# Kernel optimization log

Measured on AMD Instinct MI355X. Metric: run time of the kernel, lower is better.

## Reference

```python
import jax, jax.numpy as jnp
import numpy as np

D_MODEL = 2048
N_HEAD = 16
HEAD_DIM = D_MODEL // N_HEAD
FF_MULT = 4
LN_EPS = 1e-5


def layer_norm(x, w, b):
    mu = jnp.mean(x, axis=-1, keepdims=True)
    var = jnp.mean(jnp.square(x - mu), axis=-1, keepdims=True)
    return (x - mu) * jax.lax.rsqrt(var + LN_EPS) * w + b


def setup_inputs() -> dict:
    key = jax.random.key(0)
    ks = jax.random.split(key, 10)
    B, S, D = 2, 2048, D_MODEL
    s = 1.0 / np.sqrt(D)
    inp = {
        "x": jax.random.normal(ks[0], (B, S, D), jnp.float32),
        "token_emb": jax.random.normal(ks[1], (B, S, D), jnp.float32),
        # torch Linear weights are (out_features, in_features)
        "Wq": jax.random.normal(ks[2], (D, D), jnp.float32) * s,
        "Wk": jax.random.normal(ks[3], (D, D), jnp.float32) * s,
        "Wv": jax.random.normal(ks[4], (D, D), jnp.float32) * s,
        "Wo": jax.random.normal(ks[5], (D, D), jnp.float32) * s,
        "W1": jax.random.normal(ks[6], (FF_MULT * D, D), jnp.float32) * s,
        "W2": jax.random.normal(ks[7], (D, FF_MULT * D), jnp.float32) * (1.0 / np.sqrt(FF_MULT * D)),
        "ln1_w": jnp.ones((D,), jnp.float32),
        "ln1_b": jnp.zeros((D,), jnp.float32),
        "ln2_w": jnp.ones((D,), jnp.float32),
        "ln2_b": jnp.zeros((D,), jnp.float32),
    }
    return inp


def reference(x, token_emb, Wq, Wk, Wv, Wo, W1, W2, ln1_w, ln1_b, ln2_w, ln2_b):
    B, S, D = x.shape
    H, Hd = N_HEAD, HEAD_DIM

    h_norm = layer_norm(x, ln1_w, ln1_b)
    # torch Linear: y = x @ W.T
    q = (h_norm @ Wq.T).reshape(B, S, H, Hd).transpose(0, 2, 1, 3)  # (B,H,S,Hd)
    k = (h_norm @ Wk.T).reshape(B, S, H, Hd).transpose(0, 2, 1, 3)
    v = (token_emb @ Wv.T).reshape(B, S, H, Hd).transpose(0, 2, 1, 3)

    scores = jnp.einsum("bhqd,bhkd->bhqk", q, k) / np.sqrt(Hd)
    causal = jnp.tril(jnp.ones((S, S), bool))  # (S,S)
    scores = jnp.where(causal, scores, -jnp.inf)
    weights = jax.nn.softmax(scores, axis=-1)

    attn = jnp.einsum("bhqk,bhkd->bhqd", weights, v)
    attn = attn.transpose(0, 2, 1, 3).reshape(B, S, D)
    attn = attn @ Wo.T
    x = x + attn

    h_ffn = layer_norm(x, ln2_w, ln2_b)
    ffn = jax.nn.gelu(h_ffn @ W1.T, approximate=False) @ W2.T
    return x + ffn
```

## Files before the change

kernel.cpp:

```cpp
#include <hip/hip_runtime.h>
#include <hip/hip_bf16.h>
#include <math.h>

#define D_MODEL 2048
#define SEQ     2048
#define BATCH   2
#define NTOK    (BATCH*SEQ)
#define NHEAD   16
#define HDIM    128
#define FF      8192

typedef float  f32x4  __attribute__((ext_vector_type(4)));
typedef __bf16 bf16x8 __attribute__((ext_vector_type(8)));

__device__ __forceinline__ unsigned short f2bfbits(float f) {
    unsigned u = __builtin_bit_cast(unsigned, f);
    return (unsigned short)((u + 0x7fffu + ((u >> 16) & 1u)) >> 16);
}
__device__ __forceinline__ __bf16 f2bf(float f) {
    unsigned short h = f2bfbits(f);
    return __builtin_bit_cast(__bf16, h);
}

__device__ __forceinline__ void gld_lds16(const void* g, void* l) {
    __builtin_amdgcn_global_load_lds(
        (const __attribute__((address_space(1))) unsigned int*)g,
        (__attribute__((address_space(3))) unsigned int*)l, 16, 0, 0);
}

__global__ __launch_bounds__(256) void cvt_all(
        const float* __restrict__ tok, const float* __restrict__ wq,
        const float* __restrict__ wk,  const float* __restrict__ wv,
        const float* __restrict__ wo,  const float* __restrict__ w1,
        const float* __restrict__ w2,
        __bf16* __restrict__ tokb, __bf16* __restrict__ wqb,
        __bf16* __restrict__ wkb,  __bf16* __restrict__ wvb,
        __bf16* __restrict__ wob,  __bf16* __restrict__ w1b,
        __bf16* __restrict__ w2b) {
    const size_t M4 = 4u * 1024 * 1024;
    size_t i = (size_t)blockIdx.x * 1024 + (size_t)threadIdx.x * 4;
    const float* src; __bf16* dst; size_t off;
    if      (i < 2*M4)  { src = tok; dst = tokb; off = i; }
    else if (i < 3*M4)  { src = wq;  dst = wqb;  off = i - 2*M4; }
    else if (i < 4*M4)  { src = wk;  dst = wkb;  off = i - 3*M4; }
    else if (i < 5*M4)  { src = wv;  dst = wvb;  off = i - 4*M4; }
    else if (i < 6*M4)  { src = wo;  dst = wob;  off = i - 5*M4; }
    else if (i < 10*M4) { src = w1;  dst = w1b;  off = i - 6*M4; }
    else                { src = w2;  dst = w2b;  off = i - 10*M4; }
    float4 v = *(const float4*)(src + off);
    ushort4 o;
    o.x = f2bfbits(v.x); o.y = f2bfbits(v.y);
    o.z = f2bfbits(v.z); o.w = f2bfbits(v.w);
    *(ushort4*)((unsigned short*)dst + off) = o;
}

__global__ __launch_bounds__(256) void add_reduce(
        const float* __restrict__ p0, const float* __restrict__ p1,
        const float* __restrict__ resid, float* __restrict__ out) {
    int i = blockIdx.x * 256 + threadIdx.x;
    float4 a = ((const float4*)p0)[i];
    float4 b = ((const float4*)p1)[i];
    float4 r = ((const float4*)resid)[i];
    float4 o;
    o.x = a.x + b.x + r.x; o.y = a.y + b.y + r.y;
    o.z = a.z + b.z + r.z; o.w = a.w + b.w + r.w;
    ((float4*)out)[i] = o;
}

__global__ __launch_bounds__(256) void ln_bf16(
        const float* __restrict__ x, const float* __restrict__ w,
        const float* __restrict__ b, __bf16* __restrict__ out) {
    const int row = blockIdx.x;
    const int tid = threadIdx.x;
    const float* xr = x + (size_t)row * D_MODEL;
    float4 v0 = *(const float4*)(xr + tid * 8);
    float4 v1 = *(const float4*)(xr + tid * 8 + 4);
    float va[8] = {v0.x, v0.y, v0.z, v0.w, v1.x, v1.y, v1.z, v1.w};
    float s = 0.f, ss = 0.f;
#pragma unroll
    for (int j = 0; j < 8; ++j) { s += va[j]; ss += va[j] * va[j]; }
#pragma unroll
    for (int m = 32; m; m >>= 1) { s += __shfl_xor(s, m, 64); ss += __shfl_xor(ss, m, 64); }
    __shared__ float red[8];
    const int wid = tid >> 6;
    if ((tid & 63) == 0) { red[wid * 2] = s; red[wid * 2 + 1] = ss; }
    __syncthreads();
    s  = red[0] + red[2] + red[4] + red[6];
    ss = red[1] + red[3] + red[5] + red[7];
    const float mu   = s * (1.0f / D_MODEL);
    const float var  = ss * (1.0f / D_MODEL) - mu * mu;
    const float rstd = rsqrtf(var + 1e-5f);
    const int c = tid * 8;
    ushort4 o0, o1;
    unsigned short ob[8];
#pragma unroll
    for (int j = 0; j < 8; ++j)
        ob[j] = f2bfbits((va[j] - mu) * rstd * w[c + j] + b[c + j]);
    o0.x = ob[0]; o0.y = ob[1]; o0.z = ob[2]; o0.w = ob[3];
    o1.x = ob[4]; o1.y = ob[5]; o1.z = ob[6]; o1.w = ob[7];
    ushort4* op = (ushort4*)(out + (size_t)row * D_MODEL + c);
    op[0] = o0; op[1] = o1;
}

template <int EPI, int SPLITK>
__global__ __launch_bounds__(512, 2) void gemm_bt8(
        const __bf16* __restrict__ A, const __bf16* __restrict__ Bm,
        __bf16* __restrict__ Cb, float* __restrict__ Cf,
        const float* __restrict__ resid, int M, int N, int K) {
    __shared__ __align__(16) __bf16 lds[2][2][256 * 64];
    const int tid = threadIdx.x;
    const int wid = tid >> 6, lane = tid & 63;
    const int l16 = lane & 15, lhi = lane >> 4;
    const int wm = wid >> 2, wn = wid & 3;

    int id = blockIdx.x;
    const int cpx = gridDim.x >> 3;
    id = (id & 7) * cpx + (id >> 3);
    const int nbn = N >> 8;
    int slice = 0;
    if (SPLITK == 2) {
        const int nblk = (M >> 8) * nbn;
        slice = id / nblk;
        id -= slice * nblk;
    }
    const int bm = id / nbn, bn = id % nbn;

    const __bf16* Ag = A  + (size_t)bm * 256 * K;
    const __bf16* Bg = Bm + (size_t)bn * 256 * K;
    const int tps = (K >> 6) / SPLITK;
    const int t0 = slice * tps, t1 = t0 + tps;

    auto stage = [&](__bf16* region, const __bf16* G, int kt, int half) {
#pragma unroll
        for (int j = 0; j < 2; ++j) {
            int idx = j * 512 + tid;
            int r128 = idx >> 3;
            int Xc = (idx & 7) << 4;
            int Xs = Xc ^ ((r128 & 7) << 4);
            gld_lds16((const char*)(G + ((size_t)(half * 128 + r128) * K + kt * 64)) + Xs,
                      (char*)region + half * 16384 + idx * 16);
        }
    };

    f32x4 acc[8][4] = {};
    bf16x8 af0[4][2], af1[4][2], bq0[2][2], bq1[2][2];

    const __bf16* Abase;
    const __bf16* Bbase;
    auto ldA = [&](bf16x8 (&dst)[4][2], int qm) {
#pragma unroll
        for (int i = 0; i < 4; ++i)
#pragma unroll
            for (int ks = 0; ks < 2; ++ks) {
                int r = wm * 128 + (qm * 4 + i) * 16 + l16;
                int X = ks * 64 + lhi * 16;
                dst[i][ks] = *(const bf16x8*)((const char*)Abase + r * 128 +
                                              (X ^ ((r & 7) << 4)));
            }
    };
    auto ldB = [&](bf16x8 (&dst)[2][2], int qn) {
#pragma unroll
        for (int j = 0; j < 2; ++j)
#pragma unroll
            for (int ks = 0; ks < 2; ++ks) {
                int r = wn * 64 + (qn * 2 + j) * 16 + l16;
                int X = ks * 64 + lhi * 16;
                dst[j][ks] = *(const bf16x8*)((const char*)Bbase + r * 128 +
                                              (X ^ ((r & 7) << 4)));
            }
    };
    auto mfmaQ = [&](bf16x8 (&a)[4][2], bf16x8 (&b)[2][2], int mo, int no) {
        __builtin_amdgcn_s_setprio(1);
#pragma unroll
        for (int i = 0; i < 4; ++i)
#pragma unroll
            for (int j = 0; j < 2; ++j)
#pragma unroll
                for (int ks = 0; ks < 2; ++ks)
                    acc[mo + i][no + j] = __builtin_amdgcn_mfma_f32_16x16x32_bf16(
                        a[i][ks], b[j][ks], acc[mo + i][no + j], 0, 0, 0);
        __builtin_amdgcn_s_setprio(0);
    };

    stage(&lds[0][0][0], Ag, t0, 0); stage(&lds[0][0][0], Ag, t0, 1);
    stage(&lds[0][1][0], Bg, t0, 0); stage(&lds[0][1][0], Bg, t0, 1);
    asm volatile("s_waitcnt vmcnt(0)" ::: "memory");
    __builtin_amdgcn_s_barrier();

    for (int t = t0; t < t1; ++t) {
        const int cur = (t - t0) & 1;
        Abase = &lds[cur][0][0];
        Bbase = &lds[cur][1][0];
        const bool pf = (t + 1 < t1);
        if (pf) {
            stage(&lds[cur ^ 1][0][0], Ag, t + 1, 0);
            stage(&lds[cur ^ 1][0][0], Ag, t + 1, 1);
            stage(&lds[cur ^ 1][1][0], Bg, t + 1, 0);
            stage(&lds[cur ^ 1][1][0], Bg, t + 1, 1);
        }
        ldA(af0, 0); ldB(bq0, 0);
        __builtin_amdgcn_s_barrier();
        asm volatile("s_waitcnt lgkmcnt(0)" ::: "memory");
        __builtin_amdgcn_sched_barrier(0);
        mfmaQ(af0, bq0, 0, 0);
        __builtin_amdgcn_s_barrier();
        ldB(bq1, 1);
        __builtin_amdgcn_s_barrier();
        asm volatile("s_waitcnt lgkmcnt(0)" ::: "memory");
        __builtin_amdgcn_sched_barrier(0);
        mfmaQ(af0, bq1, 0, 2);
        __builtin_amdgcn_s_barrier();
        ldA(af1, 1);
        __builtin_amdgcn_s_barrier();
        asm volatile("s_waitcnt lgkmcnt(0)" ::: "memory");
        __builtin_amdgcn_sched_barrier(0);
        mfmaQ(af1, bq0, 4, 0);
        __builtin_amdgcn_s_barrier();
        mfmaQ(af1, bq1, 4, 2);
        if (pf) asm volatile("s_waitcnt vmcnt(0)" ::: "memory");
        __builtin_amdgcn_s_barrier();
    }

#pragma unroll
    for (int m = 0; m < 8; ++m) {
        const int row = bm * 256 + wm * 128 + m * 16 + lhi * 4;
#pragma unroll
        for (int n = 0; n < 4; ++n) {
            const int col = bn * 256 + wn * 64 + n * 16 + l16;
            if (EPI == 3) {
                const int h = col >> 7, hd = col & 127;
                const size_t obase =
                    ((((size_t)(row >> 11) * NHEAD + h) * HDIM + hd) << 11) + (row & 2047);
                ushort4 o;
                o.x = f2bfbits(acc[m][n][0]); o.y = f2bfbits(acc[m][n][1]);
                o.z = f2bfbits(acc[m][n][2]); o.w = f2bfbits(acc[m][n][3]);
                *(ushort4*)((unsigned short*)Cb + obase) = o;
            } else {
#pragma unroll
                for (int r = 0; r < 4; ++r) {
                    float v = acc[m][n][r];
                    size_t off = (size_t)(row + r) * N + col;
                    if (EPI == 0) {
                        Cb[off] = f2bf(v);
                    } else if (EPI == 1) {
                        Cb[off] = f2bf(0.5f * v * (1.0f + erff(v * 0.70710678118654752f)));
                    } else if (EPI == 2) {
                        Cf[off] = v + resid[off];
                    } else {
                        Cf[(size_t)slice * M * N + off] = v;
                    }
                }
            }
        }
    }
}

#define LDQK 4096
__global__ __launch_bounds__(256) void attn_causal(
        const __bf16* __restrict__ Q, const __bf16* __restrict__ K,
        const __bf16* __restrict__ Vt, __bf16* __restrict__ O) {
    const int qt = gridDim.x - 1 - blockIdx.x;
    const int h = blockIdx.y, bb = blockIdx.z;
    const int tid = threadIdx.x, wid = tid >> 6, lane = tid & 63;
    const int l16 = lane & 15, lhi = lane >> 4;
    __shared__ __align__(16) __bf16 Ks[64 * 128];
    __shared__ __align__(16) __bf16 Vs[128 * 64];
    __shared__ __align__(16) __bf16 Pl[4][16 * 72];

    const size_t qkbase = ((size_t)bb * SEQ) * LDQK + (size_t)h * HDIM;
    const size_t obase  = ((size_t)bb * SEQ) * D_MODEL + (size_t)h * HDIM;
    const size_t vtbase = (((size_t)bb * NHEAD + h) * HDIM) << 11;
    const int q0 = qt * 64 + wid * 16;

    bf16x8 qf[4];
#pragma unroll
    for (int ks = 0; ks < 4; ++ks)
        qf[ks] = *(const bf16x8*)(Q + qkbase + (size_t)(q0 + l16) * LDQK + ks * 32 + lhi * 8);

    f32x4 accO[8] = {};
    float m_run[4], l_run[4];
#pragma unroll
    for (int r = 0; r < 4; ++r) { m_run[r] = -1e30f; l_run[r] = 0.f; }

    const float scale2 = 0.08838834764831845f * 1.4426950408889634f;

    for (int kt = 0; kt <= qt; ++kt) {
#pragma unroll
        for (int i = 0; i < 4; ++i) {
            int idx = i * 256 + tid;
            int row = idx >> 4, c8 = idx & 15;
            int c8s = c8 ^ (row & 7);
            gld_lds16(K + qkbase + (size_t)(kt * 64 + row) * LDQK + c8s * 8, Ks + idx * 8);
        }
#pragma unroll
        for (int i = 0; i < 4; ++i) {
            int idx = i * 256 + tid;
            int row = idx >> 3, c8 = idx & 7;
            int c8s = c8 ^ (row & 7);
            gld_lds16(Vt + vtbase + (size_t)row * SEQ + kt * 64 + c8s * 8, Vs + idx * 8);
        }
        __syncthreads();

        f32x4 s[4] = {};
        __builtin_amdgcn_s_setprio(1);
#pragma unroll
        for (int nb = 0; nb < 4; ++nb) {
            const int tok = nb * 16 + l16;
#pragma unroll
            for (int ks = 0; ks < 4; ++ks) {
                int co = (ks * 64 + lhi * 16) ^ ((tok & 7) << 4);
                bf16x8 kf = *(const bf16x8*)((const char*)Ks + tok * 256 + co);
                s[nb] = __builtin_amdgcn_mfma_f32_16x16x32_bf16(qf[ks], kf, s[nb], 0, 0, 0);
            }
        }
        __builtin_amdgcn_s_setprio(0);
        const bool diag = (kt == qt);
#pragma unroll
        for (int nb = 0; nb < 4; ++nb)
#pragma unroll
            for (int r = 0; r < 4; ++r) {
                float sv = s[nb][r] * scale2;
                if (diag && (nb * 16 + l16) > (wid * 16 + lhi * 4 + r)) sv = -1e30f;
                s[nb][r] = sv;
            }
        float alpha[4];
#pragma unroll
        for (int r = 0; r < 4; ++r) {
            float mx = fmaxf(fmaxf(s[0][r], s[1][r]), fmaxf(s[2][r], s[3][r]));
#pragma unroll
            for (int m = 8; m; m >>= 1) mx = fmaxf(mx, __shfl_xor(mx, m, 64));
            float mnew = fmaxf(m_run[r], mx);
            alpha[r] = exp2f(m_run[r] - mnew);
            float rs = 0.f;
#pragma unroll
            for (int nb = 0; nb < 4; ++nb) {
                float p = exp2f(s[nb][r] - mnew);
                s[nb][r] = p;
                rs += p;
            }
#pragma unroll
            for (int m = 8; m; m >>= 1) rs += __shfl_xor(rs, m, 64);
            l_run[r] = l_run[r] * alpha[r] + rs;
            m_run[r] = mnew;
        }
#pragma unroll
        for (int d8 = 0; d8 < 8; ++d8)
#pragma unroll
            for (int r = 0; r < 4; ++r) accO[d8][r] *= alpha[r];
#pragma unroll
        for (int nb = 0; nb < 4; ++nb)
#pragma unroll
            for (int r = 0; r < 4; ++r)
                Pl[wid][(lhi * 4 + r) * 72 + nb * 16 + l16] = f2bf(s[nb][r]);
        __builtin_amdgcn_s_setprio(1);
#pragma unroll
        for (int ks2 = 0; ks2 < 2; ++ks2) {
            bf16x8 pa = *(const bf16x8*)(&Pl[wid][l16 * 72 + ks2 * 32 + lhi * 8]);
#pragma unroll
            for (int d8 = 0; d8 < 8; ++d8) {
                const int d = d8 * 16 + l16;
                const int co = ((ks2 * 4 + lhi) ^ (d & 7)) << 4;
                bf16x8 vf = *(const bf16x8*)((const char*)Vs + d * 128 + co);
                accO[d8] = __builtin_amdgcn_mfma_f32_16x16x32_bf16(pa, vf, accO[d8], 0, 0, 0);
            }
        }
        __builtin_amdgcn_s_setprio(0);
        __syncthreads();
    }

#pragma unroll
    for (int d8 = 0; d8 < 8; ++d8)
#pragma unroll
        for (int r = 0; r < 4; ++r) {
            float o = accO[d8][r] / l_run[r];
            O[obase + (size_t)(q0 + lhi * 4 + r) * D_MODEL + d8 * 16 + l16] = f2bf(o);
        }
}

extern "C" void kernel_launch(void* const* d_in, const int* in_sizes, int n_in,
                              void* d_out, int out_size, void* d_ws, size_t ws_size,
                              hipStream_t stream) {
    const float* x    = (const float*)d_in[0];
    const float* tok  = (const float*)d_in[1];
    const float* Wq   = (const float*)d_in[2];
    const float* Wk   = (const float*)d_in[3];
    const float* Wv   = (const float*)d_in[4];
    const float* Wo   = (const float*)d_in[5];
    const float* W1   = (const float*)d_in[6];
    const float* W2   = (const float*)d_in[7];
    const float* ln1w = (const float*)d_in[8];
    const float* ln1b = (const float*)d_in[9];
    const float* ln2w = (const float*)d_in[10];
    const float* ln2b = (const float*)d_in[11];
    float* out = (float*)d_out;

    char* ws = (char*)d_ws;
    size_t off = 0;
    auto alloc = [&](size_t bytes) { void* p = ws + off; off += bytes; return p; };
    __bf16* tokb  = (__bf16*)alloc((size_t)NTOK * D_MODEL * 2);
    __bf16* hnorm = (__bf16*)alloc((size_t)NTOK * D_MODEL * 2);
    __bf16* wqb   = (__bf16*)alloc((size_t)D_MODEL * D_MODEL * 2);
    __bf16* wkb   = (__bf16*)alloc((size_t)D_MODEL * D_MODEL * 2);
    __bf16* wvb   = (__bf16*)alloc((size_t)D_MODEL * D_MODEL * 2);
    __bf16* wob   = (__bf16*)alloc((size_t)D_MODEL * D_MODEL * 2);
    __bf16* w1b   = (__bf16*)alloc((size_t)FF * D_MODEL * 2);
    __bf16* w2b   = (__bf16*)alloc((size_t)D_MODEL * FF * 2);
    __bf16* QKb   = (__bf16*)alloc((size_t)NTOK * 2 * D_MODEL * 2);
    __bf16* Vtg   = (__bf16*)alloc((size_t)NTOK * D_MODEL * 2);
    __bf16* Ab    = (__bf16*)alloc((size_t)NTOK * D_MODEL * 2);
    float*  x2    = (float*)alloc((size_t)NTOK * D_MODEL * 4);
    __bf16* gb    = QKb;
    float*  p0    = (float*)(ws);
    float*  p1    = p0 + (size_t)NTOK * D_MODEL;

    cvt_all<<<56 * 1024, 256, 0, stream>>>(tok, Wq, Wk, Wv, Wo, W1, W2,
                                           tokb, wqb, wkb, wvb, wob, w1b, w2b);

    ln_bf16<<<NTOK, 256, 0, stream>>>(x, ln1w, ln1b, hnorm);

    const int g_qk = (NTOK / 256) * ((2 * D_MODEL) / 256);
    gemm_bt8<0, 1><<<g_qk, 512, 0, stream>>>(hnorm, wqb, QKb, nullptr, nullptr,
                                             NTOK, 2 * D_MODEL, D_MODEL);
    const int g_sq = (NTOK / 256) * (D_MODEL / 256);
    gemm_bt8<3, 1><<<g_sq, 512, 0, stream>>>(tokb, wvb, Vtg, nullptr, nullptr,
                                             NTOK, D_MODEL, D_MODEL);

    attn_causal<<<dim3(SEQ / 64, NHEAD, BATCH), 256, 0, stream>>>(QKb, QKb + D_MODEL, Vtg, Ab);

    gemm_bt8<2, 1><<<g_sq, 512, 0, stream>>>(Ab, wob, nullptr, x2, x, NTOK, D_MODEL, D_MODEL);

    ln_bf16<<<NTOK, 256, 0, stream>>>(x2, ln2w, ln2b, hnorm);

    const int g_ff = (NTOK / 256) * (FF / 256);
    gemm_bt8<1, 1><<<g_ff, 512, 0, stream>>>(hnorm, w1b, gb, nullptr, nullptr,
                                             NTOK, FF, D_MODEL);
    gemm_bt8<4, 2><<<2 * g_sq, 512, 0, stream>>>(gb, w2b, nullptr, p0, nullptr,
                                                 NTOK, D_MODEL, FF);
    add_reduce<<<(NTOK * D_MODEL) / 1024, 256, 0, stream>>>(p0, p1, x2, out);
}
```

Measured before the change: 760.2 us.

## Widen causal attention tile to 128 queries and double-buffer K loads

The attention kernel now runs 8 waves per block over 128 query rows, so each staged K/V tile is reused by twice as many waves. K is double-buffered and the next tile is prefetched while the current QK^T runs. V is loaded in parallel with score computation, and split waitcnt/barrier points replace the full syncthreads. Masking is decided per wave, so waves in the lower half of the tile do some extra fully masked key tiles. Halving the grid also risks worse load balance across CUs.

```diff
diff --git a/kernel.cpp b/kernel.cpp
--- a/kernel.cpp
+++ b/kernel.cpp
@@ -256,50 +256,65 @@
 }
 
 #define LDQK 4096
-__global__ __launch_bounds__(256) void attn_causal(
+__global__ __launch_bounds__(512) void attn_causal(
         const __bf16* __restrict__ Q, const __bf16* __restrict__ K,
         const __bf16* __restrict__ Vt, __bf16* __restrict__ O) {
     const int qt = gridDim.x - 1 - blockIdx.x;
     const int h = blockIdx.y, bb = blockIdx.z;
     const int tid = threadIdx.x, wid = tid >> 6, lane = tid & 63;
     const int l16 = lane & 15, lhi = lane >> 4;
-    __shared__ __align__(16) __bf16 Ks[64 * 128];
+    __shared__ __align__(16) __bf16 Ks[2][64 * 128];
     __shared__ __align__(16) __bf16 Vs[128 * 64];
-    __shared__ __align__(16) __bf16 Pl[4][16 * 72];
+    __shared__ __align__(16) __bf16 Pl[8][16 * 72];
 
     const size_t qkbase = ((size_t)bb * SEQ) * LDQK + (size_t)h * HDIM;
     const size_t obase  = ((size_t)bb * SEQ) * D_MODEL + (size_t)h * HDIM;
     const size_t vtbase = (((size_t)bb * NHEAD + h) * HDIM) << 11;
-    const int q0 = qt * 64 + wid * 16;
+    const int q0 = qt * 128 + wid * 16;
 
     bf16x8 qf[4];
 #pragma unroll
     for (int ks = 0; ks < 4; ++ks)
         qf[ks] = *(const bf16x8*)(Q + qkbase + (size_t)(q0 + l16) * LDQK + ks * 32 + lhi * 8);
 
-    f32x4 accO[8] = {};
-    float m_run[4], l_run[4];
-#pragma unroll
-    for (int r = 0; r < 4; ++r) { m_run[r] = -1e30f; l_run[r] = 0.f; }
-
-    const float scale2 = 0.08838834764831845f * 1.4426950408889634f;
-
-    for (int kt = 0; kt <= qt; ++kt) {
-#pragma unroll
-        for (int i = 0; i < 4; ++i) {
-            int idx = i * 256 + tid;
+    auto stageK = [&](int kt, int buf) {
+#pragma unroll
+        for (int j = 0; j < 2; ++j) {
+            int idx = j * 512 + tid;
             int row = idx >> 4, c8 = idx & 15;
             int c8s = c8 ^ (row & 7);
-            gld_lds16(K + qkbase + (size_t)(kt * 64 + row) * LDQK + c8s * 8, Ks + idx * 8);
-        }
-#pragma unroll
-        for (int i = 0; i < 4; ++i) {
-            int idx = i * 256 + tid;
+            gld_lds16(K + qkbase + (size_t)(kt * 64 + row) * LDQK + c8s * 8,
+                      &Ks[buf][0] + idx * 8);
+        }
+    };
+    auto stageV = [&](int kt) {
+#pragma unroll
+        for (int j = 0; j < 2; ++j) {
+            int idx = j * 512 + tid;
             int row = idx >> 3, c8 = idx & 7;
             int c8s = c8 ^ (row & 7);
             gld_lds16(Vt + vtbase + (size_t)row * SEQ + kt * 64 + c8s * 8, Vs + idx * 8);
         }
-        __syncthreads();
+    };
+
+    f32x4 accO[8] = {};
+    float m_run[4], l_run[4];
+#pragma unroll
+    for (int r = 0; r < 4; ++r) { m_run[r] = -1e30f; l_run[r] = 0.f; }
+
+    const float scale2 = 0.08838834764831845f * 1.4426950408889634f;
+    const int NKT = (qt + 1) * 2;
+
+    stageK(0, 0);
+    asm volatile("s_waitcnt vmcnt(0)" ::: "memory");
+    __builtin_amdgcn_s_barrier();
+    __builtin_amdgcn_sched_barrier(0);
+
+    for (int kt = 0; kt < NKT; ++kt) {
+        const int cb = kt & 1;
+        const bool pf = (kt + 1 < NKT);
+        stageV(kt);
+        if (pf) stageK(kt + 1, cb ^ 1);
 
         f32x4 s[4] = {};
         __builtin_amdgcn_s_setprio(1);
@@ -309,20 +324,28 @@
 #pragma unroll
             for (int ks = 0; ks < 4; ++ks) {
                 int co = (ks * 64 + lhi * 16) ^ ((tok & 7) << 4);
-                bf16x8 kf = *(const bf16x8*)((const char*)Ks + tok * 256 + co);
+                bf16x8 kf = *(const bf16x8*)((const char*)&Ks[cb][0] + tok * 256 + co);
                 s[nb] = __builtin_amdgcn_mfma_f32_16x16x32_bf16(qf[ks], kf, s[nb], 0, 0, 0);
             }
         }
         __builtin_amdgcn_s_setprio(0);
-        const bool diag = (kt == qt);
-#pragma unroll
-        for (int nb = 0; nb < 4; ++nb)
-#pragma unroll
-            for (int r = 0; r < 4; ++r) {
-                float sv = s[nb][r] * scale2;
-                if (diag && (nb * 16 + l16) > (wid * 16 + lhi * 4 + r)) sv = -1e30f;
-                s[nb][r] = sv;
-            }
+
+        if (((kt + 1) << 6) > q0) {
+#pragma unroll
+            for (int nb = 0; nb < 4; ++nb)
+#pragma unroll
+                for (int r = 0; r < 4; ++r) {
+                    float sv = s[nb][r] * scale2;
+                    if ((kt * 64 + nb * 16 + l16) > (q0 + lhi * 4 + r)) sv = -1e30f;
+                    s[nb][r] = sv;
+                }
+        } else {
+#pragma unroll
+            for (int nb = 0; nb < 4; ++nb)
+#pragma unroll
+                for (int r = 0; r < 4; ++r) s[nb][r] *= scale2;
+        }
+
         float alpha[4];
 #pragma unroll
         for (int r = 0; r < 4; ++r) {
@@ -352,6 +375,12 @@
 #pragma unroll
             for (int r = 0; r < 4; ++r)
                 Pl[wid][(lhi * 4 + r) * 72 + nb * 16 + l16] = f2bf(s[nb][r]);
+
+        if (pf) asm volatile("s_waitcnt vmcnt(2)" ::: "memory");
+        else    asm volatile("s_waitcnt vmcnt(0)" ::: "memory");
+        __builtin_amdgcn_s_barrier();
+        __builtin_amdgcn_sched_barrier(0);
+
         __builtin_amdgcn_s_setprio(1);
 #pragma unroll
         for (int ks2 = 0; ks2 < 2; ++ks2) {
@@ -365,7 +394,10 @@
             }
         }
         __builtin_amdgcn_s_setprio(0);
-        __syncthreads();
+
+        asm volatile("s_waitcnt vmcnt(0)" ::: "memory");
+        __builtin_amdgcn_s_barrier();
+        __builtin_amdgcn_sched_barrier(0);
     }
 
 #pragma unroll
@@ -425,7 +457,7 @@
     gemm_bt8<3, 1><<<g_sq, 512, 0, stream>>>(tokb, wvb, Vtg, nullptr, nullptr,
                                              NTOK, D_MODEL, D_MODEL);
 
-    attn_causal<<<dim3(SEQ / 64, NHEAD, BATCH), 256, 0, stream>>>(QKb, QKb + D_MODEL, Vtg, Ab);
+    attn_causal<<<dim3(SEQ / 128, NHEAD, BATCH), 512, 0, stream>>>(QKb, QKb + D_MODEL, Vtg, Ab);
 
     gemm_bt8<2, 1><<<g_sq, 512, 0, stream>>>(Ab, wob, nullptr, x2, x, NTOK, D_MODEL, D_MODEL);
 
```

Result: faster. 721.9 us (-5.0%).
